# Kernel tuning notes

Measured on AMD Instinct MI355X. Metric: run time of the kernel, lower is better.

Reference implementation:

```python
import jax, jax.numpy as jnp
import numpy as np

B, HID, NH = 2048, 512, 8
HD = HID // NH


def _slstm(x, W, b, R, h, c):
    # gates = W_gates(x) + R_gates(h); chunk order i,f,g,o
    g = x @ W.T + b + h @ R.T
    i, f, gg, o = jnp.split(g, 4, axis=1)
    c_new = jax.nn.sigmoid(f) * c + jnp.exp(i) * jnp.tanh(gg)
    return jax.nn.sigmoid(o) * jnp.tanh(c_new)


def _mlstm(x, Wq, bq, Wk, bk, Wv, bv, igw, igb, fgw, fgb, lng, lnb):
    Bsz = x.shape[0]
    q = (x @ Wq.T + bq).reshape(Bsz, NH, HD)
    k = (x @ Wk.T + bk).reshape(Bsz, NH, HD)
    v = (x @ Wv.T + bv).reshape(Bsz, NH, HD)
    i = jnp.exp(x @ igw.T + igb)            # [B,H] input gate (exponential)
    f = jax.nn.sigmoid(x @ fgw.T + fgb)     # [B,H]; multiplies zero init state -> drops out
    # initial state (C, n, m) is zeros, so C_new = i * (v k^T), n_new = i * v, m_new = i
    C = i[:, :, None, None] * (v[..., :, None] * k[..., None, :])  # [B,H,hd,hd]
    n = i[:, :, None] * v                                          # [B,H,hd]
    m = i                                                          # [B,H]
    num = jnp.einsum('bhij,bhj->bhi', C, q)
    den = jnp.einsum('bhi,bhi->bh', n, q) + m + 1e-6
    h = (num / den[..., None]).reshape(Bsz, HID)
    mu = h.mean(-1, keepdims=True)
    var = ((h - mu) ** 2).mean(-1, keepdims=True)
    return (h - mu) / jnp.sqrt(var + 1e-5) * lng + lnb


def setup_inputs() -> dict:
    key = jax.random.key(0)
    ks = iter(jax.random.split(key, 64))
    rn = lambda shape, s: jax.random.normal(next(ks), shape, dtype=jnp.float32) * s
    inp = {
        'V': jax.random.normal(next(ks), (B, 1), dtype=jnp.float32),
        't': jax.random.uniform(next(ks), (B, 1), dtype=jnp.float32),
        'ip_w': rn((HID, 2), 0.1), 'ip_b': rn((HID,), 0.02),
        'op_w': rn((1, HID), 0.05), 'op_b': rn((1,), 0.02),
    }
    for p in ('s0', 's2'):
        inp[p + '_W'] = rn((4 * HID, HID), 0.05)
        inp[p + '_b'] = rn((4 * HID,), 0.05)
        inp[p + '_R'] = rn((4 * HID, HID), 0.05)
    for p in ('m1', 'm3'):
        for nm in ('Wq', 'Wk', 'Wv'):
            inp[p + '_' + nm] = rn((HID, HID), 0.05)
        for nm in ('bq', 'bk', 'bv'):
            inp[p + '_' + nm] = rn((HID,), 0.02)
        inp[p + '_igw'] = rn((NH, HID), 0.05)
        inp[p + '_igb'] = rn((NH,), 0.1)
        inp[p + '_fgw'] = rn((NH, HID), 0.05)
        inp[p + '_fgb'] = jnp.linspace(3.0, 6.0, NH, dtype=jnp.float32)
        inp[p + '_lng'] = jnp.ones((HID,), dtype=jnp.float32)
        inp[p + '_lnb'] = jnp.zeros((HID,), dtype=jnp.float32)
    return inp


def reference(V, t, ip_w, ip_b, op_w, op_b,
              s0_W, s0_b, s0_R, s2_W, s2_b, s2_R,
              m1_Wq, m1_Wk, m1_Wv, m1_bq, m1_bk, m1_bv,
              m1_igw, m1_igb, m1_fgw, m1_fgb, m1_lng, m1_lnb,
              m3_Wq, m3_Wk, m3_Wv, m3_bq, m3_bk, m3_bv,
              m3_igw, m3_igb, m3_fgw, m3_fgb, m3_lng, m3_lnb):
    x = jnp.concatenate([V, t], axis=1)           # [B,2]
    h = x @ ip_w.T + ip_b                         # [B,HID]
    z = jnp.zeros((h.shape[0], HID), h.dtype)
    h = _slstm(h, s0_W, s0_b, s0_R, z, z)         # layer 0: sLSTM
    h = _mlstm(h, m1_Wq, m1_bq, m1_Wk, m1_bk, m1_Wv, m1_bv,
               m1_igw, m1_igb, m1_fgw, m1_fgb, m1_lng, m1_lnb)  # layer 1: mLSTM
    h = _slstm(h, s2_W, s2_b, s2_R, z, z)         # layer 2: sLSTM
    h = _mlstm(h, m3_Wq, m3_bq, m3_Wk, m3_bk, m3_Wv, m3_bv,
               m3_igw, m3_igb, m3_fgw, m3_fgb, m3_lng, m3_lnb)  # layer 3: mLSTM
    return h @ op_w.T + op_b                      # I_pred [B,1]
```

## Files before the change

### kernel.cpp

```cpp
#include <hip/hip_runtime.h>
#include <hip/hip_bf16.h>

#define HID 512
#define BATCH 2048

typedef __bf16 bf16x8 __attribute__((ext_vector_type(8)));
typedef float f32x4 __attribute__((ext_vector_type(4)));
typedef float f32x16 __attribute__((ext_vector_type(16)));
typedef __hip_bfloat16 bf16;

__device__ inline unsigned short f2bf(float x) {
    bf16 h = __float2bfloat16(x);
    return __builtin_bit_cast(unsigned short, h);
}
__device__ inline float bf2f(unsigned short u) {
    return __bfloat162float(__builtin_bit_cast(bf16, u));
}

__device__ inline void gload16(const void* g, void* l) {
    __builtin_amdgcn_global_load_lds((const __attribute__((address_space(1))) void*)g,
                                     (__attribute__((address_space(3))) void*)l, 16, 0, 0);
}

struct CvtArgs { const float* src[7]; };

__global__ void k_prep(CvtArgs a, unsigned short* __restrict__ hi, unsigned short* __restrict__ lo,
                       const float* __restrict__ s0W, const float* __restrict__ s0b,
                       const float* __restrict__ ipw, const float* __restrict__ ipb,
                       float* __restrict__ uV, float* __restrict__ uT, float* __restrict__ uC) {
    const int bid = blockIdx.x;
    if (bid < 2560) {
        int idx4 = (bid * 256 + threadIdx.x) << 2;
        int seg, off; size_t dst;
        if (idx4 < 1048576) { seg = 0; off = idx4; dst = 1048576 + idx4; }
        else { int r = idx4 - 1048576; seg = 1 + (r >> 18); off = r & 262143; dst = 2097152 + r; }
        f32x4 w = *(const f32x4*)(a.src[seg] + off);
        ushort4 h, l;
        h.x = f2bf(w[0]); h.y = f2bf(w[1]); h.z = f2bf(w[2]); h.w = f2bf(w[3]);
        l.x = f2bf(w[0] - bf2f(h.x)); l.y = f2bf(w[1] - bf2f(h.y));
        l.z = f2bf(w[2] - bf2f(h.z)); l.w = f2bf(w[3] - bf2f(h.w));
        *(ushort4*)(hi + dst) = h;
        *(ushort4*)(lo + dst) = l;
    } else {
        const int w = threadIdx.x >> 6, lane = threadIdx.x & 63;
        const int r = (bid - 2560) * 4 + w;
        const int wr = r < 512 ? r : r + 512;
        const float* Wp = s0W + (size_t)wr * HID + lane * 8;
        f32x4 wa = *(const f32x4*)Wp, wb = *(const f32x4*)(Wp + 4);
        const float* pw = ipw + lane * 16;
        f32x4 e0 = *(const f32x4*)pw,       e1 = *(const f32x4*)(pw + 4);
        f32x4 e2 = *(const f32x4*)(pw + 8), e3 = *(const f32x4*)(pw + 12);
        f32x4 ba = *(const f32x4*)(ipb + lane * 8), bb = *(const f32x4*)(ipb + lane * 8 + 4);
        float s0 = wa[0]*e0[0] + wa[1]*e0[2] + wa[2]*e1[0] + wa[3]*e1[2]
                 + wb[0]*e2[0] + wb[1]*e2[2] + wb[2]*e3[0] + wb[3]*e3[2];
        float s1 = wa[0]*e0[1] + wa[1]*e0[3] + wa[2]*e1[1] + wa[3]*e1[3]
                 + wb[0]*e2[1] + wb[1]*e2[3] + wb[2]*e3[1] + wb[3]*e3[3];
        float s2 = wa[0]*ba[0] + wa[1]*ba[1] + wa[2]*ba[2] + wa[3]*ba[3]
                 + wb[0]*bb[0] + wb[1]*bb[1] + wb[2]*bb[2] + wb[3]*bb[3];
#pragma unroll
        for (int off = 32; off; off >>= 1) {
            s0 += __shfl_xor(s0, off); s1 += __shfl_xor(s1, off); s2 += __shfl_xor(s2, off);
        }
        if (lane == 0) { uV[r] = s0; uT[r] = s1; uC[r] = s2 + s0b[wr]; }
    }
}

__global__ void k_slstm0(const float* __restrict__ V, const float* __restrict__ t,
                         const float* __restrict__ uV, const float* __restrict__ uT,
                         const float* __restrict__ uC,
                         unsigned short* __restrict__ hhi, unsigned short* __restrict__ hlo) {
    int idx = blockIdx.x * blockDim.x + threadIdx.x;
    int b = idx >> 7, j4 = (idx & 127) << 2;
    float vv = V[b], tt = t[b];
    f32x4 gi = vv * *(const f32x4*)(uV + j4)        + tt * *(const f32x4*)(uT + j4)        + *(const f32x4*)(uC + j4);
    f32x4 gg = vv * *(const f32x4*)(uV + 512 + j4)  + tt * *(const f32x4*)(uT + 512 + j4)  + *(const f32x4*)(uC + 512 + j4);
    f32x4 go = vv * *(const f32x4*)(uV + 1024 + j4) + tt * *(const f32x4*)(uT + 1024 + j4) + *(const f32x4*)(uC + 1024 + j4);
    ushort4 h, l;
    float x[4];
#pragma unroll
    for (int u = 0; u < 4; ++u)
        x[u] = tanhf(expf(gi[u]) * tanhf(gg[u])) / (1.f + expf(-go[u]));
    h.x = f2bf(x[0]); h.y = f2bf(x[1]); h.z = f2bf(x[2]); h.w = f2bf(x[3]);
    l.x = f2bf(x[0] - bf2f(h.x)); l.y = f2bf(x[1] - bf2f(h.y));
    l.z = f2bf(x[2] - bf2f(h.z)); l.w = f2bf(x[3] - bf2f(h.w));
    size_t o = (size_t)b * HID + j4;
    *(ushort4*)(hhi + o) = h;
    *(ushort4*)(hlo + o) = l;
}

__global__ __launch_bounds__(256, 2) void k_gemm(
    const bf16* __restrict__ Ahi, const bf16* __restrict__ Alo,
    const bf16* __restrict__ Wh0, const bf16* __restrict__ Wh1, const bf16* __restrict__ Wh2,
    const bf16* __restrict__ Wl0, const bf16* __restrict__ Wl1, const bf16* __restrict__ Wl2,
    float* __restrict__ C)
{
    __shared__ __align__(16) bf16 lds[5][8192];
    const int tid = threadIdx.x, w = tid >> 6, lane = tid & 63;

    const int bid = blockIdx.x;
    const int xcd = bid & 7, slot = bid >> 3;
    const int m0 = (xcd * 2 + slot / 12) * 128;
    const int n0 = (slot % 12) * 128;
    const int nseg = n0 >> 9, nloc = n0 & 511;
    const bf16* Wh = nseg == 0 ? Wh0 : (nseg == 1 ? Wh1 : Wh2);
    const bf16* Wl = nseg == 0 ? Wl0 : (nseg == 1 ? Wl1 : Wl2);

    const bf16* msrc = (w == 0) ? Ahi : (w == 1) ? Alo : (w == 2) ? Wh : Wl;
    const int rowbase = (w < 2) ? m0 : nloc;
    const size_t srow = (size_t)(rowbase + (lane & 31)) * HID + ((lane >> 5) << 3);

    auto STAGE = [&](int t) {
        bf16* db = &lds[t % 5][0] + (w << 11) + (lane << 3);
        const bf16* gp = msrc + srow + (t << 4);
#pragma unroll
        for (int p = 0; p < 4; ++p)
            gload16(gp + (size_t)(p << 5) * HID, db + (p << 9));
    };

    const int wm = w >> 1, wn = w & 1;
    const int la = lane << 3;
    f32x16 acc00 = {}, acc01 = {}, acc10 = {}, acc11 = {};

    STAGE(0); STAGE(1); STAGE(2); STAGE(3);
#pragma unroll
    for (int t = 0; t < 32; ++t) {
        if (t < 29)
            asm volatile("s_waitcnt vmcnt(12) lgkmcnt(0)\n\ts_barrier" ::: "memory");
        else if (t == 29)
            asm volatile("s_waitcnt vmcnt(8) lgkmcnt(0)\n\ts_barrier" ::: "memory");
        else if (t == 30)
            asm volatile("s_waitcnt vmcnt(4) lgkmcnt(0)\n\ts_barrier" ::: "memory");
        else
            asm volatile("s_waitcnt vmcnt(0) lgkmcnt(0)\n\ts_barrier" ::: "memory");
        if (t < 28) STAGE(t + 4);
        const bf16* lb = &lds[t % 5][0];
        bf16x8 ah0 = *(const bf16x8*)(lb + ((2 * wm    ) << 9) + la);
        bf16x8 ah1 = *(const bf16x8*)(lb + ((2 * wm + 1) << 9) + la);
        bf16x8 al0 = *(const bf16x8*)(lb + ((4 + 2 * wm    ) << 9) + la);
        bf16x8 al1 = *(const bf16x8*)(lb + ((4 + 2 * wm + 1) << 9) + la);
        bf16x8 wh0 = *(const bf16x8*)(lb + ((8 + 2 * wn    ) << 9) + la);
        bf16x8 wh1 = *(const bf16x8*)(lb + ((8 + 2 * wn + 1) << 9) + la);
        bf16x8 wl0 = *(const bf16x8*)(lb + ((12 + 2 * wn    ) << 9) + la);
        bf16x8 wl1 = *(const bf16x8*)(lb + ((12 + 2 * wn + 1) << 9) + la);
        acc00 = __builtin_amdgcn_mfma_f32_32x32x16_bf16(ah0, wh0, acc00, 0, 0, 0);
        acc01 = __builtin_amdgcn_mfma_f32_32x32x16_bf16(ah0, wh1, acc01, 0, 0, 0);
        acc10 = __builtin_amdgcn_mfma_f32_32x32x16_bf16(ah1, wh0, acc10, 0, 0, 0);
        acc11 = __builtin_amdgcn_mfma_f32_32x32x16_bf16(ah1, wh1, acc11, 0, 0, 0);
        acc00 = __builtin_amdgcn_mfma_f32_32x32x16_bf16(al0, wh0, acc00, 0, 0, 0);
        acc01 = __builtin_amdgcn_mfma_f32_32x32x16_bf16(al0, wh1, acc01, 0, 0, 0);
        acc10 = __builtin_amdgcn_mfma_f32_32x32x16_bf16(al1, wh0, acc10, 0, 0, 0);
        acc11 = __builtin_amdgcn_mfma_f32_32x32x16_bf16(al1, wh1, acc11, 0, 0, 0);
        acc00 = __builtin_amdgcn_mfma_f32_32x32x16_bf16(ah0, wl0, acc00, 0, 0, 0);
        acc01 = __builtin_amdgcn_mfma_f32_32x32x16_bf16(ah0, wl1, acc01, 0, 0, 0);
        acc10 = __builtin_amdgcn_mfma_f32_32x32x16_bf16(ah1, wl0, acc10, 0, 0, 0);
        acc11 = __builtin_amdgcn_mfma_f32_32x32x16_bf16(ah1, wl1, acc11, 0, 0, 0);
    }

    const f32x16* accs[2][2] = { { &acc00, &acc01 }, { &acc10, &acc11 } };
#pragma unroll
    for (int fi = 0; fi < 2; ++fi)
#pragma unroll
        for (int fj = 0; fj < 2; ++fj) {
            const f32x16& ac = *accs[fi][fj];
            const int col = n0 + ((2 * wn + fj) << 5) + (lane & 31);
            const int rbase = m0 + ((2 * wm + fi) << 5) + ((lane >> 5) << 2);
#pragma unroll
            for (int rr = 0; rr < 16; ++rr) {
                int row = rbase + (rr & 3) + ((rr >> 2) << 3);
                C[(size_t)row * 1536 + col] = ac[rr];
            }
        }
}

__global__ void k_slstm_act(const float* __restrict__ g, const float* __restrict__ bp,
                            unsigned short* __restrict__ hhi, unsigned short* __restrict__ hlo) {
    int idx = blockIdx.x * blockDim.x + threadIdx.x;
    int b = idx >> 7, j4 = (idx & 127) << 2;
    const float* r0 = g + (size_t)b * 1536 + j4;
    f32x4 gi = *(const f32x4*)r0 + *(const f32x4*)(bp + j4);
    f32x4 gg = *(const f32x4*)(r0 + 512) + *(const f32x4*)(bp + 1024 + j4);
    f32x4 go = *(const f32x4*)(r0 + 1024) + *(const f32x4*)(bp + 1536 + j4);
    ushort4 h, l;
    float x[4];
#pragma unroll
    for (int u = 0; u < 4; ++u)
        x[u] = tanhf(expf(gi[u]) * tanhf(gg[u])) / (1.f + expf(-go[u]));
    h.x = f2bf(x[0]); h.y = f2bf(x[1]); h.z = f2bf(x[2]); h.w = f2bf(x[3]);
    l.x = f2bf(x[0] - bf2f(h.x)); l.y = f2bf(x[1] - bf2f(h.y));
    l.z = f2bf(x[2] - bf2f(h.z)); l.w = f2bf(x[3] - bf2f(h.w));
    size_t o = (size_t)b * HID + j4;
    *(ushort4*)(hhi + o) = h;
    *(ushort4*)(hlo + o) = l;
}

__global__ __launch_bounds__(512) void k_mlstm(
    const float* __restrict__ g0,
    const float* __restrict__ bq, const float* __restrict__ bk, const float* __restrict__ bv,
    const bf16* __restrict__ hinh, const bf16* __restrict__ hinl,
    const float* __restrict__ igw, const float* __restrict__ igb,
    const float* __restrict__ lng, const float* __restrict__ lnb,
    unsigned short* __restrict__ outh, unsigned short* __restrict__ outl,
    const float* __restrict__ opw, const float* __restrict__ opb, float* __restrict__ out)
{
    int b = blockIdx.x;
    int tid = threadIdx.x, head = tid >> 6, lane = tid & 63;

    const bf16*  hh = hinh + (size_t)b * HID;
    const bf16*  hl = hinl + (size_t)b * HID;
    const float* wrow = igw + head * HID;
    float s = 0.f;
#pragma unroll
    for (int k = 0; k < 8; ++k) {
        int p = lane + 64 * k;
        s += wrow[p] * (__bfloat162float(hh[p]) + __bfloat162float(hl[p]));
    }
#pragma unroll
    for (int off = 32; off; off >>= 1) s += __shfl_xor(s, off);
    float ig = expf(s + igb[head]);

    const float* r0 = g0 + (size_t)b * 1536;
    float q  = r0[tid] + bq[tid];
    float kk = r0[512 + tid] + bk[tid];
    float v  = r0[1024 + tid] + bv[tid];
    float kq = kk * q, vq = v * q;
#pragma unroll
    for (int off = 32; off; off >>= 1) { kq += __shfl_xor(kq, off); vq += __shfl_xor(vq, off); }
    float den = ig * (vq + 1.0f) + 1e-6f;
    float hv  = v * (ig * kq) / den;

    __shared__ float red[16];
    __shared__ float red2[8];
    float s1 = hv, s2 = hv * hv;
#pragma unroll
    for (int off = 32; off; off >>= 1) { s1 += __shfl_xor(s1, off); s2 += __shfl_xor(s2, off); }
    if (lane == 0) { red[head] = s1; red[8 + head] = s2; }
    __syncthreads();
    float t1 = 0.f, t2 = 0.f;
#pragma unroll
    for (int h2 = 0; h2 < 8; ++h2) { t1 += red[h2]; t2 += red[8 + h2]; }
    float mu  = t1 * (1.f / 512.f);
    float var = t2 * (1.f / 512.f) - mu * mu;
    float o = (hv - mu) * rsqrtf(var + 1e-5f) * lng[tid] + lnb[tid];

    if (out) {
        float po = o * opw[tid];
#pragma unroll
        for (int off = 32; off; off >>= 1) po += __shfl_xor(po, off);
        if (lane == 0) red2[head] = po;
        __syncthreads();
        if (tid == 0) {
            float tt = 0.f;
#pragma unroll
            for (int h2 = 0; h2 < 8; ++h2) tt += red2[h2];
            out[b] = tt + opb[0];
        }
    } else {
        unsigned short oh = f2bf(o);
        size_t p = (size_t)b * HID + tid;
        outh[p] = oh;
        outl[p] = f2bf(o - bf2f(oh));
    }
}

extern "C" void kernel_launch(void* const* d_in, const int* in_sizes, int n_in,
                              void* d_out, int out_size, void* d_ws, size_t ws_size,
                              hipStream_t stream) {
    const float* V    = (const float*)d_in[0];
    const float* t    = (const float*)d_in[1];
    const float* ip_w = (const float*)d_in[2];
    const float* ip_b = (const float*)d_in[3];
    const float* op_w = (const float*)d_in[4];
    const float* op_b = (const float*)d_in[5];
    const float* s0_W = (const float*)d_in[6];
    const float* s0_b = (const float*)d_in[7];
    const float* s2_W = (const float*)d_in[9];
    const float* s2_b = (const float*)d_in[10];
    const float* m1_Wq = (const float*)d_in[12];
    const float* m1_Wk = (const float*)d_in[13];
    const float* m1_Wv = (const float*)d_in[14];
    const float* m1_bq = (const float*)d_in[15];
    const float* m1_bk = (const float*)d_in[16];
    const float* m1_bv = (const float*)d_in[17];
    const float* m1_igw = (const float*)d_in[18];
    const float* m1_igb = (const float*)d_in[19];
    const float* m1_lng = (const float*)d_in[22];
    const float* m1_lnb = (const float*)d_in[23];
    const float* m3_Wq = (const float*)d_in[24];
    const float* m3_Wk = (const float*)d_in[25];
    const float* m3_Wv = (const float*)d_in[26];
    const float* m3_bq = (const float*)d_in[27];
    const float* m3_bk = (const float*)d_in[28];
    const float* m3_bv = (const float*)d_in[29];
    const float* m3_igw = (const float*)d_in[30];
    const float* m3_igb = (const float*)d_in[31];
    const float* m3_lng = (const float*)d_in[34];
    const float* m3_lnb = (const float*)d_in[35];

    char* ws = (char*)d_ws;
    bf16* whi  = (bf16*)ws;
    bf16* wlo  = (bf16*)(ws + 7340032);
    bf16* hAhi = (bf16*)(ws + 14680064);
    bf16* hAlo = (bf16*)(ws + 16777216);
    bf16* hBhi = (bf16*)(ws + 18874368);
    bf16* hBlo = (bf16*)(ws + 20971520);
    float* gq  = (float*)(ws + 23068672);
    float* uV  = (float*)(ws + 35651584);
    float* uT  = uV + 1536;
    float* uC  = uT + 1536;

    CvtArgs ca;
    ca.src[0] = s2_W;
    ca.src[1] = m1_Wq; ca.src[2] = m1_Wk; ca.src[3] = m1_Wv;
    ca.src[4] = m3_Wq; ca.src[5] = m3_Wk; ca.src[6] = m3_Wv;
    k_prep<<<2944, 256, 0, stream>>>(ca, (unsigned short*)whi, (unsigned short*)wlo,
                                     s0_W, s0_b, ip_w, ip_b, uV, uT, uC);

    k_slstm0<<<1024, 256, 0, stream>>>(V, t, uV, uT, uC,
                                       (unsigned short*)hBhi, (unsigned short*)hBlo);
    k_gemm<<<192, 256, 0, stream>>>(hBhi, hBlo,
        whi + 2097152, whi + 2359296, whi + 2621440,
        wlo + 2097152, wlo + 2359296, wlo + 2621440, gq);
    k_mlstm<<<BATCH, 512, 0, stream>>>(gq, m1_bq, m1_bk, m1_bv, hBhi, hBlo,
                                       m1_igw, m1_igb, m1_lng, m1_lnb,
                                       (unsigned short*)hAhi, (unsigned short*)hAlo,
                                       nullptr, nullptr, nullptr);
    k_gemm<<<192, 256, 0, stream>>>(hAhi, hAlo,
        whi + 1048576, whi + 1572864, whi + 1835008,
        wlo + 1048576, wlo + 1572864, wlo + 1835008, gq);
    k_slstm_act<<<1024, 256, 0, stream>>>(gq, s2_b, (unsigned short*)hBhi, (unsigned short*)hBlo);
    k_gemm<<<192, 256, 0, stream>>>(hBhi, hBlo,
        whi + 2883584, whi + 3145728, whi + 3407872,
        wlo + 2883584, wlo + 3145728, wlo + 3407872, gq);
    k_mlstm<<<BATCH, 512, 0, stream>>>(gq, m3_bq, m3_bk, m3_bv, hBhi, hBlo,
                                       m3_igw, m3_igb, m3_lng, m3_lnb,
                                       nullptr, nullptr,
                                       op_w, op_b, (float*)d_out);
}
```

Baseline: 102.0 us.

## Split GEMM tile across eight waves with 512-thread blocks

The bf16x3 GEMM kernel moves from 4 waves per 128x128 tile to 8 waves, so each wave computes a 32x64 sub-tile with two accumulators instead of four. The global-to-LDS staging is spread over 8 waves at two loads each, and the vmcnt waits are adjusted to match. This is meant to hide latency better and raise per-CU wave count, since only 192 blocks run on 256 CUs. In exchange there are more LDS reads per MFMA, because the A fragments are loaded by more waves, and barriers now span more waves.

After: 101.5 us. No clear change (-0.5%).

```diff
diff --git a/kernel.cpp b/kernel.cpp
--- a/kernel.cpp
+++ b/kernel.cpp
@@ -88,7 +88,7 @@
     *(ushort4*)(hlo + o) = l;
 }
 
-__global__ __launch_bounds__(256, 2) void k_gemm(
+__global__ __launch_bounds__(512) void k_gemm(
     const bf16* __restrict__ Ahi, const bf16* __restrict__ Alo,
     const bf16* __restrict__ Wh0, const bf16* __restrict__ Wh1, const bf16* __restrict__ Wh2,
     const bf16* __restrict__ Wl0, const bf16* __restrict__ Wl1, const bf16* __restrict__ Wl2,
@@ -105,71 +105,71 @@
     const bf16* Wh = nseg == 0 ? Wh0 : (nseg == 1 ? Wh1 : Wh2);
     const bf16* Wl = nseg == 0 ? Wl0 : (nseg == 1 ? Wl1 : Wl2);
 
-    const bf16* msrc = (w == 0) ? Ahi : (w == 1) ? Alo : (w == 2) ? Wh : Wl;
-    const int rowbase = (w < 2) ? m0 : nloc;
-    const size_t srow = (size_t)(rowbase + (lane & 31)) * HID + ((lane >> 5) << 3);
+    auto src_of = [&](int c) -> const bf16* {
+        const int m = c >> 2, rb = c & 3;
+        const bf16* base = (m == 0) ? Ahi : (m == 1) ? Alo : (m == 2) ? Wh : Wl;
+        const int rowbase = (m < 2) ? m0 : nloc;
+        return base + (size_t)(rowbase + (rb << 5) + (lane & 31)) * HID + ((lane >> 5) << 3);
+    };
+    const int c0 = 2 * w;
+    const bf16* sp0 = src_of(c0);
+    const bf16* sp1 = src_of(c0 + 1);
+    bf16* const d0 = &lds[0][0] + (c0 << 9) + (lane << 3);
 
     auto STAGE = [&](int t) {
-        bf16* db = &lds[t % 5][0] + (w << 11) + (lane << 3);
-        const bf16* gp = msrc + srow + (t << 4);
-#pragma unroll
-        for (int p = 0; p < 4; ++p)
-            gload16(gp + (size_t)(p << 5) * HID, db + (p << 9));
+        bf16* db = d0 + (t % 5) * 8192;
+        gload16(sp0 + (t << 4), db);
+        gload16(sp1 + (t << 4), db + 512);
     };
 
     const int wm = w >> 1, wn = w & 1;
     const int la = lane << 3;
-    f32x16 acc00 = {}, acc01 = {}, acc10 = {}, acc11 = {};
+    const int cA  = wm << 9;
+    const int cAl = (4 + wm) << 9;
+    const int cW0 = (8 + 2 * wn) << 9;
+    const int cW1 = (9 + 2 * wn) << 9;
+    const int cL0 = (12 + 2 * wn) << 9;
+    const int cL1 = (13 + 2 * wn) << 9;
+    f32x16 acc0 = {}, acc1 = {};
 
     STAGE(0); STAGE(1); STAGE(2); STAGE(3);
 #pragma unroll
     for (int t = 0; t < 32; ++t) {
         if (t < 29)
-            asm volatile("s_waitcnt vmcnt(12) lgkmcnt(0)\n\ts_barrier" ::: "memory");
+            asm volatile("s_waitcnt vmcnt(6) lgkmcnt(0)\n\ts_barrier" ::: "memory");
         else if (t == 29)
-            asm volatile("s_waitcnt vmcnt(8) lgkmcnt(0)\n\ts_barrier" ::: "memory");
+            asm volatile("s_waitcnt vmcnt(4) lgkmcnt(0)\n\ts_barrier" ::: "memory");
         else if (t == 30)
-            asm volatile("s_waitcnt vmcnt(4) lgkmcnt(0)\n\ts_barrier" ::: "memory");
+            asm volatile("s_waitcnt vmcnt(2) lgkmcnt(0)\n\ts_barrier" ::: "memory");
         else
             asm volatile("s_waitcnt vmcnt(0) lgkmcnt(0)\n\ts_barrier" ::: "memory");
         if (t < 28) STAGE(t + 4);
         const bf16* lb = &lds[t % 5][0];
-        bf16x8 ah0 = *(const bf16x8*)(lb + ((2 * wm    ) << 9) + la);
-        bf16x8 ah1 = *(const bf16x8*)(lb + ((2 * wm + 1) << 9) + la);
-        bf16x8 al0 = *(const bf16x8*)(lb + ((4 + 2 * wm    ) << 9) + la);
-        bf16x8 al1 = *(const bf16x8*)(lb + ((4 + 2 * wm + 1) << 9) + la);
-        bf16x8 wh0 = *(const bf16x8*)(lb + ((8 + 2 * wn    ) << 9) + la);
-        bf16x8 wh1 = *(const bf16x8*)(lb + ((8 + 2 * wn + 1) << 9) + la);
-        bf16x8 wl0 = *(const bf16x8*)(lb + ((12 + 2 * wn    ) << 9) + la);
-        bf16x8 wl1 = *(const bf16x8*)(lb + ((12 + 2 * wn + 1) << 9) + la);
-        acc00 = __builtin_amdgcn_mfma_f32_32x32x16_bf16(ah0, wh0, acc00, 0, 0, 0);
-        acc01 = __builtin_amdgcn_mfma_f32_32x32x16_bf16(ah0, wh1, acc01, 0, 0, 0);
-        acc10 = __builtin_amdgcn_mfma_f32_32x32x16_bf16(ah1, wh0, acc10, 0, 0, 0);
-        acc11 = __builtin_amdgcn_mfma_f32_32x32x16_bf16(ah1, wh1, acc11, 0, 0, 0);
-        acc00 = __builtin_amdgcn_mfma_f32_32x32x16_bf16(al0, wh0, acc00, 0, 0, 0);
-        acc01 = __builtin_amdgcn_mfma_f32_32x32x16_bf16(al0, wh1, acc01, 0, 0, 0);
-        acc10 = __builtin_amdgcn_mfma_f32_32x32x16_bf16(al1, wh0, acc10, 0, 0, 0);
-        acc11 = __builtin_amdgcn_mfma_f32_32x32x16_bf16(al1, wh1, acc11, 0, 0, 0);
-        acc00 = __builtin_amdgcn_mfma_f32_32x32x16_bf16(ah0, wl0, acc00, 0, 0, 0);
-        acc01 = __builtin_amdgcn_mfma_f32_32x32x16_bf16(ah0, wl1, acc01, 0, 0, 0);
-        acc10 = __builtin_amdgcn_mfma_f32_32x32x16_bf16(ah1, wl0, acc10, 0, 0, 0);
-        acc11 = __builtin_amdgcn_mfma_f32_32x32x16_bf16(ah1, wl1, acc11, 0, 0, 0);
-    }
-
-    const f32x16* accs[2][2] = { { &acc00, &acc01 }, { &acc10, &acc11 } };
-#pragma unroll
-    for (int fi = 0; fi < 2; ++fi)
-#pragma unroll
-        for (int fj = 0; fj < 2; ++fj) {
-            const f32x16& ac = *accs[fi][fj];
-            const int col = n0 + ((2 * wn + fj) << 5) + (lane & 31);
-            const int rbase = m0 + ((2 * wm + fi) << 5) + ((lane >> 5) << 2);
-#pragma unroll
-            for (int rr = 0; rr < 16; ++rr) {
-                int row = rbase + (rr & 3) + ((rr >> 2) << 3);
-                C[(size_t)row * 1536 + col] = ac[rr];
-            }
+        bf16x8 ah  = *(const bf16x8*)(lb + cA  + la);
+        bf16x8 al  = *(const bf16x8*)(lb + cAl + la);
+        bf16x8 wh0 = *(const bf16x8*)(lb + cW0 + la);
+        bf16x8 wh1 = *(const bf16x8*)(lb + cW1 + la);
+        bf16x8 wl0 = *(const bf16x8*)(lb + cL0 + la);
+        bf16x8 wl1 = *(const bf16x8*)(lb + cL1 + la);
+        acc0 = __builtin_amdgcn_mfma_f32_32x32x16_bf16(ah, wh0, acc0, 0, 0, 0);
+        acc1 = __builtin_amdgcn_mfma_f32_32x32x16_bf16(ah, wh1, acc1, 0, 0, 0);
+        acc0 = __builtin_amdgcn_mfma_f32_32x32x16_bf16(al, wh0, acc0, 0, 0, 0);
+        acc1 = __builtin_amdgcn_mfma_f32_32x32x16_bf16(al, wh1, acc1, 0, 0, 0);
+        acc0 = __builtin_amdgcn_mfma_f32_32x32x16_bf16(ah, wl0, acc0, 0, 0, 0);
+        acc1 = __builtin_amdgcn_mfma_f32_32x32x16_bf16(ah, wl1, acc1, 0, 0, 0);
+    }
+
+    const int rb4 = (lane >> 5) << 2;
+#pragma unroll
+    for (int f = 0; f < 2; ++f) {
+        const f32x16& ac = f ? acc1 : acc0;
+        const int col = n0 + ((2 * wn + f) << 5) + (lane & 31);
+#pragma unroll
+        for (int rr = 0; rr < 16; ++rr) {
+            int row = m0 + (wm << 5) + (rr & 3) + ((rr >> 2) << 3) + rb4;
+            C[(size_t)row * 1536 + col] = ac[rr];
         }
+    }
 }
 
 __global__ void k_slstm_act(const float* __restrict__ g, const float* __restrict__ bp,
@@ -317,18 +317,18 @@
 
     k_slstm0<<<1024, 256, 0, stream>>>(V, t, uV, uT, uC,
                                        (unsigned short*)hBhi, (unsigned short*)hBlo);
-    k_gemm<<<192, 256, 0, stream>>>(hBhi, hBlo,
+    k_gemm<<<192, 512, 0, stream>>>(hBhi, hBlo,
         whi + 2097152, whi + 2359296, whi + 2621440,
         wlo + 2097152, wlo + 2359296, wlo + 2621440, gq);
     k_mlstm<<<BATCH, 512, 0, stream>>>(gq, m1_bq, m1_bk, m1_bv, hBhi, hBlo,
                                        m1_igw, m1_igb, m1_lng, m1_lnb,
                                        (unsigned short*)hAhi, (unsigned short*)hAlo,
                                        nullptr, nullptr, nullptr);
-    k_gemm<<<192, 256, 0, stream>>>(hAhi, hAlo,
+    k_gemm<<<192, 512, 0, stream>>>(hAhi, hAlo,
         whi + 1048576, whi + 1572864, whi + 1835008,
         wlo + 1048576, wlo + 1572864, wlo + 1835008, gq);
     k_slstm_act<<<1024, 256, 0, stream>>>(gq, s2_b, (unsigned short*)hBhi, (unsigned short*)hBlo);
-    k_gemm<<<192, 256, 0, stream>>>(hBhi, hBlo,
+    k_gemm<<<192, 512, 0, stream>>>(hBhi, hBlo,
         whi + 2883584, whi + 3145728, whi + 3407872,
         wlo + 2883584, wlo + 3145728, wlo + 3407872, gq);
     k_mlstm<<<BATCH, 512, 0, stream>>>(gq, m3_bq, m3_bk, m3_bv, hBhi, hBlo,
```
